# Optimization experiments

Hardware: AMD Instinct MI355X
Metric: run time of the kernel (lower is better)

## Reference

```python
import jax, jax.numpy as jnp
import numpy as np

B, L, H, NUM_LABELS = 4, 256, 768, 13


def setup_inputs() -> dict:
    key = jax.random.key(0)
    k1, k2, k3, k4, k5 = jax.random.split(key, 5)
    s1 = 1.0 / np.sqrt(2 * H)
    s2 = 1.0 / np.sqrt(H)
    return {
        "hidden_states": jax.random.normal(k1, (B, L, H), dtype=jnp.float32),
        "W1": jax.random.uniform(k2, (2 * H, H), jnp.float32, -s1, s1),
        "b1": jax.random.uniform(k3, (H,), jnp.float32, -s1, s1),
        "W2": jax.random.uniform(k4, (H, NUM_LABELS), jnp.float32, -s2, s2),
        "b2": jax.random.uniform(k5, (NUM_LABELS,), jnp.float32, -s2, s2),
    }


def reference(hidden_states, W1, b1, W2, b2):
    # Original: ffn(cat([x_start expand over dim2, x_end expand over dim1], -1))
    # Algebraically: Linear(2H->H) on the concat == proj(x_start) + proj(x_end)
    # broadcast over the L x L span grid, avoiding the (B,L,L,2H) tensor.
    H_ = hidden_states.shape[-1]
    xs_proj = jnp.einsum('bsh,hk->bsk', hidden_states, W1[:H_])   # start half
    xe_proj = jnp.einsum('bsh,hk->bsk', hidden_states, W1[H_:])   # end half
    h = xs_proj[:, :, None, :] + xe_proj[:, None, :, :] + b1      # (B,L,L,H)
    h = jax.nn.gelu(h, approximate=False)                         # torch GELU default = exact erf
    logits = jnp.einsum('bijk,kn->bijn', h, W2) + b2              # (B,L,L,num_labels)
    return logits
```

## Files before the change

### kernel.cpp

```cpp
#include <hip/hip_runtime.h>
#include <math.h>

#define H 768
#define L 256
#define NB 4
#define NL 13

typedef _Float16 h2 __attribute__((ext_vector_type(2)));
typedef _Float16 h4 __attribute__((ext_vector_type(4)));
typedef _Float16 half8 __attribute__((ext_vector_type(8)));
typedef float f32x4 __attribute__((ext_vector_type(4)));

__device__ inline unsigned int h2const(float f) {
    _Float16 c = (_Float16)f;
    h2 r = {c, c};
    return __builtin_bit_cast(unsigned int, r);
}

__device__ inline void gelu4_asm(
    unsigned int xs0, unsigned int xs1, unsigned int xs2, unsigned int xs3,
    unsigned int xe0, unsigned int xe1, unsigned int xe2, unsigned int xe3,
    unsigned int lo, unsigned int hi,
    unsigned int d4, unsigned int d3, unsigned int d2, unsigned int d1,
    unsigned int d0,
    unsigned int& o0r, unsigned int& o1r, unsigned int& o2r, unsigned int& o3r)
{
    unsigned int o0, o1, o2, o3, c0, c1, c2, c3, u0, u1, u2, u3, p0, p1, p2, p3;
    asm("v_pk_add_f16 %[o0], %[xs0], %[xe0]\n\t"
        "v_pk_add_f16 %[o1], %[xs1], %[xe1]\n\t"
        "v_pk_add_f16 %[o2], %[xs2], %[xe2]\n\t"
        "v_pk_add_f16 %[o3], %[xs3], %[xe3]\n\t"
        "v_pk_max_f16 %[c0], %[o0], %[lo]\n\t"
        "v_pk_max_f16 %[c1], %[o1], %[lo]\n\t"
        "v_pk_max_f16 %[c2], %[o2], %[lo]\n\t"
        "v_pk_max_f16 %[c3], %[o3], %[lo]\n\t"
        "v_pk_min_f16 %[c0], %[c0], %[hi]\n\t"
        "v_pk_min_f16 %[c1], %[c1], %[hi]\n\t"
        "v_pk_min_f16 %[c2], %[c2], %[hi]\n\t"
        "v_pk_min_f16 %[c3], %[c3], %[hi]\n\t"
        "v_pk_mul_f16 %[u0], %[c0], %[c0]\n\t"
        "v_pk_mul_f16 %[u1], %[c1], %[c1]\n\t"
        "v_pk_mul_f16 %[u2], %[c2], %[c2]\n\t"
        "v_pk_mul_f16 %[u3], %[c3], %[c3]\n\t"
        "v_pk_fma_f16 %[p0], %[u0], %[d4], %[d3]\n\t"
        "v_pk_fma_f16 %[p1], %[u1], %[d4], %[d3]\n\t"
        "v_pk_fma_f16 %[p2], %[u2], %[d4], %[d3]\n\t"
        "v_pk_fma_f16 %[p3], %[u3], %[d4], %[d3]\n\t"
        "v_pk_fma_f16 %[p0], %[u0], %[p0], %[d2]\n\t"
        "v_pk_fma_f16 %[p1], %[u1], %[p1], %[d2]\n\t"
        "v_pk_fma_f16 %[p2], %[u2], %[p2], %[d2]\n\t"
        "v_pk_fma_f16 %[p3], %[u3], %[p3], %[d2]\n\t"
        "v_pk_fma_f16 %[p0], %[u0], %[p0], %[d1]\n\t"
        "v_pk_fma_f16 %[p1], %[u1], %[p1], %[d1]\n\t"
        "v_pk_fma_f16 %[p2], %[u2], %[p2], %[d1]\n\t"
        "v_pk_fma_f16 %[p3], %[u3], %[p3], %[d1]\n\t"
        "v_pk_fma_f16 %[p0], %[u0], %[p0], %[d0]\n\t"
        "v_pk_fma_f16 %[p1], %[u1], %[p1], %[d0]\n\t"
        "v_pk_fma_f16 %[p2], %[u2], %[p2], %[d0]\n\t"
        "v_pk_fma_f16 %[p3], %[u3], %[p3], %[d0]\n\t"
        "v_pk_mul_f16 %[p0], %[c0], %[p0]\n\t"
        "v_pk_mul_f16 %[p1], %[c1], %[p1]\n\t"
        "v_pk_mul_f16 %[p2], %[c2], %[p2]\n\t"
        "v_pk_mul_f16 %[p3], %[c3], %[p3]\n\t"
        "v_pk_fma_f16 %[o0], %[o0], %[p0], %[o0]\n\t"
        "v_pk_fma_f16 %[o1], %[o1], %[p1], %[o1]\n\t"
        "v_pk_fma_f16 %[o2], %[o2], %[p2], %[o2]\n\t"
        "v_pk_fma_f16 %[o3], %[o3], %[p3], %[o3]"
        : [o0]"=&v"(o0), [o1]"=&v"(o1), [o2]"=&v"(o2), [o3]"=&v"(o3),
          [c0]"=&v"(c0), [c1]"=&v"(c1), [c2]"=&v"(c2), [c3]"=&v"(c3),
          [u0]"=&v"(u0), [u1]"=&v"(u1), [u2]"=&v"(u2), [u3]"=&v"(u3),
          [p0]"=&v"(p0), [p1]"=&v"(p1), [p2]"=&v"(p2), [p3]"=&v"(p3)
        : [xs0]"v"(xs0), [xs1]"v"(xs1), [xs2]"v"(xs2), [xs3]"v"(xs3),
          [xe0]"v"(xe0), [xe1]"v"(xe1), [xe2]"v"(xe2), [xe3]"v"(xe3),
          [lo]"v"(lo), [hi]"v"(hi), [d4]"v"(d4), [d3]"v"(d3),
          [d2]"v"(d2), [d1]"v"(d1), [d0]"v"(d0));
    o0r = o0; o1r = o1; o2r = o2; o3r = o3;
}

__global__ __launch_bounds__(256) void gemm_fused(
    const float* __restrict__ X, const float* __restrict__ W1,
    const float* __restrict__ b1, const float* __restrict__ W2,
    _Float16* __restrict__ Pxs2, _Float16* __restrict__ Pxe,
    _Float16* __restrict__ Bfrag2)
{
    const int tid = threadIdx.x;

    if (blockIdx.x >= 768) {
        int base = (blockIdx.x - 768) * 768 + tid;
        #pragma unroll
        for (int r = 0; r < 3; ++r) {
            int idx = base + r * 256;
            int u = idx & 7;
            int lane = (idx >> 3) & 63;
            int kb = idx >> 9;
            int k = kb * 32 + ((lane >> 4) << 3) + u;
            int nn = lane & 15;
            float v = (nn < NL) ? W2[(size_t)k * NL + nn] : 0.f;
            Bfrag2[idx] = (_Float16)(0.5f * v);
        }
        return;
    }

    __shared__ _Float16 As[2][32][72];
    __shared__ _Float16 Bs[2][64][72];

    const int w = tid >> 6, lane = tid & 63;
    const int ln = lane & 15, quad = lane >> 4;
    const int bm = blockIdx.x & 31;
    const int bn = blockIdx.x >> 5;
    const int m0 = bm * 32;
    const int n0g = bn * 64;
    const bool isE = (n0g >= H);
    const float* Wb = W1 + (isE ? (size_t)H * H : 0);
    const int c0 = isE ? (n0g - H) : n0g;

    const int ar = tid >> 4;
    const int ac = (tid & 15) * 4;

    float4 fA0, fA1, fB0a, fB0b, fB1a, fB1b;

#define G_LOAD(KR) do { \
    const int k0_ = (KR) * 64; \
    fA0 = *(const float4*)&X[(size_t)(m0 + ar) * H + k0_ + ac]; \
    fA1 = *(const float4*)&X[(size_t)(m0 + 16 + ar) * H + k0_ + ac]; \
    const float* wr0_ = &Wb[(size_t)(k0_ + 2 * ar) * H + c0 + ac]; \
    fB0a = *(const float4*)wr0_; \
    fB0b = *(const float4*)(wr0_ + H); \
    const float* wr1_ = &Wb[(size_t)(k0_ + 2 * (16 + ar)) * H + c0 + ac]; \
    fB1a = *(const float4*)wr1_; \
    fB1b = *(const float4*)(wr1_ + H); \
} while (0)

#define L_STORE(BUF) do { \
    h4 oa0 = { (_Float16)fA0.x, (_Float16)fA0.y, (_Float16)fA0.z, (_Float16)fA0.w }; \
    h4 oa1 = { (_Float16)fA1.x, (_Float16)fA1.y, (_Float16)fA1.z, (_Float16)fA1.w }; \
    *(h4*)&As[BUF][ar][ac] = oa0; \
    *(h4*)&As[BUF][16 + ar][ac] = oa1; \
    h2 p0 = {(_Float16)fB0a.x, (_Float16)fB0b.x}; \
    h2 p1 = {(_Float16)fB0a.y, (_Float16)fB0b.y}; \
    h2 p2 = {(_Float16)fB0a.z, (_Float16)fB0b.z}; \
    h2 p3 = {(_Float16)fB0a.w, (_Float16)fB0b.w}; \
    *(h2*)&Bs[BUF][ac + 0][2 * ar] = p0; \
    *(h2*)&Bs[BUF][ac + 1][2 * ar] = p1; \
    *(h2*)&Bs[BUF][ac + 2][2 * ar] = p2; \
    *(h2*)&Bs[BUF][ac + 3][2 * ar] = p3; \
    h2 q0 = {(_Float16)fB1a.x, (_Float16)fB1b.x}; \
    h2 q1 = {(_Float16)fB1a.y, (_Float16)fB1b.y}; \
    h2 q2 = {(_Float16)fB1a.z, (_Float16)fB1b.z}; \
    h2 q3 = {(_Float16)fB1a.w, (_Float16)fB1b.w}; \
    *(h2*)&Bs[BUF][ac + 0][2 * (16 + ar)] = q0; \
    *(h2*)&Bs[BUF][ac + 1][2 * (16 + ar)] = q1; \
    *(h2*)&Bs[BUF][ac + 2][2 * (16 + ar)] = q2; \
    *(h2*)&Bs[BUF][ac + 3][2 * (16 + ar)] = q3; \
} while (0)

    const int wm = w & 1, wn = w >> 1;
    f32x4 acc[2] = {};

    G_LOAD(0);
    L_STORE(0);
    __syncthreads();

    for (int kr = 0; kr < 12; ++kr) {
        const int cur = kr & 1;
        if (kr < 11) G_LOAD(kr + 1);
        #pragma unroll
        for (int sub = 0; sub < 2; ++sub) {
            const int ko = sub * 32 + quad * 8;
            half8 a   = *(const half8*)&As[cur][wm * 16 + ln][ko];
            half8 b0  = *(const half8*)&Bs[cur][wn * 32 + ln][ko];
            half8 b1f = *(const half8*)&Bs[cur][wn * 32 + 16 + ln][ko];
            acc[0] = __builtin_amdgcn_mfma_f32_16x16x32_f16(a, b0,  acc[0], 0, 0, 0);
            acc[1] = __builtin_amdgcn_mfma_f32_16x16x32_f16(a, b1f, acc[1], 0, 0, 0);
        }
        if (kr < 11) L_STORE(cur ^ 1);
        __syncthreads();
    }

    const int mb = m0 + wm * 16 + quad * 4;
    const int nb = wn * 32;
    if (!isE) {
        float bv0 = b1[n0g + nb + ln];
        float bv1 = b1[n0g + nb + 16 + ln];
        #pragma unroll
        for (int r = 0; r < 4; ++r) {
            Pxs2[(size_t)(mb + r) * H + (n0g + nb + ln)]      = (_Float16)(acc[0][r] + bv0);
            Pxs2[(size_t)(mb + r) * H + (n0g + nb + 16 + ln)] = (_Float16)(acc[1][r] + bv1);
        }
    } else {
        #pragma unroll
        for (int r = 0; r < 4; ++r) {
            Pxe[(size_t)(mb + r) * H + (c0 + nb + ln)]      = (_Float16)acc[0][r];
            Pxe[(size_t)(mb + r) * H + (c0 + nb + 16 + ln)] = (_Float16)acc[1][r];
        }
    }
#undef G_LOAD
#undef L_STORE
}

__global__ __launch_bounds__(256, 4) void span_mfma_kernel(
    const _Float16* __restrict__ Pxs2, const _Float16* __restrict__ Pxe,
    const _Float16* __restrict__ Bfrag2, const float* __restrict__ b2,
    float* __restrict__ out)
{
    __shared__ unsigned int xsf[4 * H / 2];
    const int ip = blockIdx.x >> 2;
    const int jq = blockIdx.x & 3;
    const int bi0 = ip * 4;
    const int b = bi0 >> 8;
    const int tid = threadIdx.x;

    const unsigned int* xsrc = (const unsigned int*)(Pxs2 + (size_t)bi0 * H);
    #pragma unroll
    for (int t = 0; t < 6; ++t) xsf[t * 256 + tid] = xsrc[t * 256 + tid];

    const int wave = tid >> 6;
    const int lane = tid & 63;
    const int n = lane & 15;
    const int quad = lane >> 4;
    const int j_load = jq * 64 + wave * 16 + n;

    const _Float16* xerow = Pxe + (size_t)(b * L + j_load) * H + quad * 8;
    const uint4* bptr = (const uint4*)(Bfrag2 + (size_t)lane * 8);

    unsigned int cLo = h2const(-3.75f), cHi = h2const(3.75f);
    unsigned int cD4 = h2const(2.0333e-5f), cD3 = h2const(-0.00084672f);
    unsigned int cD2 = h2const(0.0140002f), cD1 = h2const(-0.1234557f);
    unsigned int cD0 = h2const(0.7946463f);
    asm("" : "+v"(cLo), "+v"(cHi), "+v"(cD4), "+v"(cD3),
             "+v"(cD2), "+v"(cD1), "+v"(cD0));

    f32x4 acc[4] = {};
    __syncthreads();

    uint4 xe0 = *(const uint4*)(xerow);
    uint4 xe1 = *(const uint4*)(xerow + 32);
    uint4 bf0 = bptr[0];
    uint4 bf1 = bptr[64];

    const int xob = quad * 4;
    uint4 xa0 = *(const uint4*)&xsf[0 * (H / 2) + xob];
    uint4 xa1 = *(const uint4*)&xsf[1 * (H / 2) + xob];
    uint4 xa2 = *(const uint4*)&xsf[2 * (H / 2) + xob];
    uint4 xa3 = *(const uint4*)&xsf[3 * (H / 2) + xob];

    #pragma unroll 2
    for (int kb = 0; kb < H / 32; ++kb) {
        uint4 xecur = xe0;  xe0 = xe1;
        uint4 bfcur = bf0;  bf0 = bf1;
        if (kb < H / 32 - 2) {
            xe1 = *(const uint4*)(xerow + (kb + 2) * 32);
            bf1 = bptr[(kb + 2) * 64];
        }

        uint4 nx0 = xa0, nx1 = xa1, nx2 = xa2, nx3 = xa3;
        if (kb < H / 32 - 1) {
            const int xon = (kb + 1) * 16 + quad * 4;
            nx0 = *(const uint4*)&xsf[0 * (H / 2) + xon];
            nx1 = *(const uint4*)&xsf[1 * (H / 2) + xon];
            nx2 = *(const uint4*)&xsf[2 * (H / 2) + xon];
            nx3 = *(const uint4*)&xsf[3 * (H / 2) + xon];
        }

        half8 bfrag = __builtin_bit_cast(half8, bfcur);
        unsigned int pk0, pk1, pk2, pk3;

        gelu4_asm(xa0.x, xa0.y, xa0.z, xa0.w,
                  xecur.x, xecur.y, xecur.z, xecur.w,
                  cLo, cHi, cD4, cD3, cD2, cD1, cD0, pk0, pk1, pk2, pk3);
        { uint4 pk4 = {pk0, pk1, pk2, pk3};
          acc[0] = __builtin_amdgcn_mfma_f32_16x16x32_f16(
                       __builtin_bit_cast(half8, pk4), bfrag, acc[0], 0, 0, 0); }

        gelu4_asm(xa1.x, xa1.y, xa1.z, xa1.w,
                  xecur.x, xecur.y, xecur.z, xecur.w,
                  cLo, cHi, cD4, cD3, cD2, cD1, cD0, pk0, pk1, pk2, pk3);
        { uint4 pk4 = {pk0, pk1, pk2, pk3};
          acc[1] = __builtin_amdgcn_mfma_f32_16x16x32_f16(
                       __builtin_bit_cast(half8, pk4), bfrag, acc[1], 0, 0, 0); }

        gelu4_asm(xa2.x, xa2.y, xa2.z, xa2.w,
                  xecur.x, xecur.y, xecur.z, xecur.w,
                  cLo, cHi, cD4, cD3, cD2, cD1, cD0, pk0, pk1, pk2, pk3);
        { uint4 pk4 = {pk0, pk1, pk2, pk3};
          acc[2] = __builtin_amdgcn_mfma_f32_16x16x32_f16(
                       __builtin_bit_cast(half8, pk4), bfrag, acc[2], 0, 0, 0); }

        gelu4_asm(xa3.x, xa3.y, xa3.z, xa3.w,
                  xecur.x, xecur.y, xecur.z, xecur.w,
                  cLo, cHi, cD4, cD3, cD2, cD1, cD0, pk0, pk1, pk2, pk3);
        { uint4 pk4 = {pk0, pk1, pk2, pk3};
          acc[3] = __builtin_amdgcn_mfma_f32_16x16x32_f16(
                       __builtin_bit_cast(half8, pk4), bfrag, acc[3], 0, 0, 0); }

        xa0 = nx0; xa1 = nx1; xa2 = nx2; xa3 = nx3;
    }

    if (n < NL) {
        float b2v = b2[n];
        #pragma unroll
        for (int i01 = 0; i01 < 4; ++i01)
            #pragma unroll
            for (int r = 0; r < 4; ++r) {
                int j = jq * 64 + wave * 16 + quad * 4 + r;
                out[((size_t)(bi0 + i01) * L + j) * NL + n] = acc[i01][r] + b2v;
            }
    }
}

extern "C" void kernel_launch(void* const* d_in, const int* in_sizes, int n_in,
                              void* d_out, int out_size, void* d_ws, size_t ws_size,
                              hipStream_t stream)
{
    (void)in_sizes; (void)n_in; (void)out_size; (void)ws_size;
    const float* X  = (const float*)d_in[0];
    const float* W1 = (const float*)d_in[1];
    const float* b1 = (const float*)d_in[2];
    const float* W2 = (const float*)d_in[3];
    const float* b2 = (const float*)d_in[4];
    float* out = (float*)d_out;

    char* ws = (char*)d_ws;
    _Float16* Pxs2   = (_Float16*)ws;
    _Float16* Pxe    = Pxs2 + (size_t)NB * L * H;
    _Float16* Bfrag2 = Pxe + (size_t)NB * L * H;

    gemm_fused<<<dim3(784), 256, 0, stream>>>(X, W1, b1, W2, Pxs2, Pxe, Bfrag2);
    span_mfma_kernel<<<NB * L, 256, 0, stream>>>(Pxs2, Pxe, Bfrag2, b2, out);
}
```

Before: 119.5 us.

## Fuse GEMM and span kernels into one cooperative launch with grid sync

```diff
diff --git a/kernel.cpp b/kernel.cpp
--- a/kernel.cpp
+++ b/kernel.cpp
@@ -1,5 +1,8 @@
 #include <hip/hip_runtime.h>
+#include <hip/hip_cooperative_groups.h>
 #include <math.h>
+
+namespace cg = cooperative_groups;
 
 #define H 768
 #define L 256
@@ -77,47 +80,6 @@
     o0r = o0; o1r = o1; o2r = o2; o3r = o3;
 }
 
-__global__ __launch_bounds__(256) void gemm_fused(
-    const float* __restrict__ X, const float* __restrict__ W1,
-    const float* __restrict__ b1, const float* __restrict__ W2,
-    _Float16* __restrict__ Pxs2, _Float16* __restrict__ Pxe,
-    _Float16* __restrict__ Bfrag2)
-{
-    const int tid = threadIdx.x;
-
-    if (blockIdx.x >= 768) {
-        int base = (blockIdx.x - 768) * 768 + tid;
-        #pragma unroll
-        for (int r = 0; r < 3; ++r) {
-            int idx = base + r * 256;
-            int u = idx & 7;
-            int lane = (idx >> 3) & 63;
-            int kb = idx >> 9;
-            int k = kb * 32 + ((lane >> 4) << 3) + u;
-            int nn = lane & 15;
-            float v = (nn < NL) ? W2[(size_t)k * NL + nn] : 0.f;
-            Bfrag2[idx] = (_Float16)(0.5f * v);
-        }
-        return;
-    }
-
-    __shared__ _Float16 As[2][32][72];
-    __shared__ _Float16 Bs[2][64][72];
-
-    const int w = tid >> 6, lane = tid & 63;
-    const int ln = lane & 15, quad = lane >> 4;
-    const int bm = blockIdx.x & 31;
-    const int bn = blockIdx.x >> 5;
-    const int m0 = bm * 32;
-    const int n0g = bn * 64;
-    const bool isE = (n0g >= H);
-    const float* Wb = W1 + (isE ? (size_t)H * H : 0);
-    const int c0 = isE ? (n0g - H) : n0g;
-
-    const int ar = tid >> 4;
-    const int ac = (tid & 15) * 4;
-
-    float4 fA0, fA1, fB0a, fB0b, fB1a, fB1b;
 
 #define G_LOAD(KR) do { \
     const int k0_ = (KR) * 64; \
@@ -154,6 +116,45 @@
     *(h2*)&Bs[BUF][ac + 3][2 * (16 + ar)] = q3; \
 } while (0)
 
+__device__ __forceinline__ void gemm_phase(
+    int wid, int tid,
+    const float* __restrict__ X, const float* __restrict__ W1,
+    const float* __restrict__ b1, const float* __restrict__ W2,
+    _Float16* __restrict__ Pxs2, _Float16* __restrict__ Pxe,
+    _Float16* __restrict__ Bfrag2,
+    _Float16 (*As)[32][72], _Float16 (*Bs)[64][72])
+{
+    if (wid >= 768) {
+        int base = (wid - 768) * 768 + tid;
+        #pragma unroll
+        for (int r = 0; r < 3; ++r) {
+            int idx = base + r * 256;
+            int u = idx & 7;
+            int lane = (idx >> 3) & 63;
+            int kb = idx >> 9;
+            int k = kb * 32 + ((lane >> 4) << 3) + u;
+            int nn = lane & 15;
+            float v = (nn < NL) ? W2[(size_t)k * NL + nn] : 0.f;
+            Bfrag2[idx] = (_Float16)(0.5f * v);
+        }
+        return;
+    }
+
+    const int w = tid >> 6, lane = tid & 63;
+    const int ln = lane & 15, quad = lane >> 4;
+    const int bm = wid & 31;
+    const int bn = wid >> 5;
+    const int m0 = bm * 32;
+    const int n0g = bn * 64;
+    const bool isE = (n0g >= H);
+    const float* Wb = W1 + (isE ? (size_t)H * H : 0);
+    const int c0 = isE ? (n0g - H) : n0g;
+
+    const int ar = tid >> 4;
+    const int ac = (tid & 15) * 4;
+
+    float4 fA0, fA1, fB0a, fB0b, fB1a, fB1b;
+
     const int wm = w & 1, wn = w >> 1;
     f32x4 acc[2] = {};
 
@@ -194,21 +195,18 @@
             Pxe[(size_t)(mb + r) * H + (c0 + nb + 16 + ln)] = (_Float16)acc[1][r];
         }
     }
-#undef G_LOAD
-#undef L_STORE
-}
-
-__global__ __launch_bounds__(256, 4) void span_mfma_kernel(
+}
+
+__device__ __forceinline__ void span_phase(
+    int bid, int tid,
     const _Float16* __restrict__ Pxs2, const _Float16* __restrict__ Pxe,
     const _Float16* __restrict__ Bfrag2, const float* __restrict__ b2,
-    float* __restrict__ out)
-{
-    __shared__ unsigned int xsf[4 * H / 2];
-    const int ip = blockIdx.x >> 2;
-    const int jq = blockIdx.x & 3;
+    float* __restrict__ out, unsigned int* xsf)
+{
+    const int ip = bid >> 2;
+    const int jq = bid & 3;
     const int bi0 = ip * 4;
     const int b = bi0 >> 8;
-    const int tid = threadIdx.x;
 
     const unsigned int* xsrc = (const unsigned int*)(Pxs2 + (size_t)bi0 * H);
     #pragma unroll
@@ -308,6 +306,50 @@
     }
 }
 
+__global__ __launch_bounds__(256, 4) void fused_kernel(
+    const float* __restrict__ X, const float* __restrict__ W1,
+    const float* __restrict__ b1, const float* __restrict__ W2,
+    const float* __restrict__ b2,
+    _Float16* __restrict__ Pxs2, _Float16* __restrict__ Pxe,
+    _Float16* __restrict__ Bfrag2, float* __restrict__ out)
+{
+    __shared__ __align__(16) unsigned char smem[27648];
+    _Float16 (*As)[32][72] = reinterpret_cast<_Float16(*)[32][72]>(smem);
+    _Float16 (*Bs)[64][72] = reinterpret_cast<_Float16(*)[64][72]>(smem + 9216);
+    unsigned int* xsf = reinterpret_cast<unsigned int*>(smem);
+
+    const int tid = threadIdx.x;
+    const int bid = blockIdx.x;
+
+    if (bid < 784)
+        gemm_phase(bid, tid, X, W1, b1, W2, Pxs2, Pxe, Bfrag2, As, Bs);
+
+    cg::this_grid().sync();
+
+    span_phase(bid, tid, Pxs2, Pxe, Bfrag2, b2, out, xsf);
+}
+
+__global__ __launch_bounds__(256) void gemm_fused(
+    const float* __restrict__ X, const float* __restrict__ W1,
+    const float* __restrict__ b1, const float* __restrict__ W2,
+    _Float16* __restrict__ Pxs2, _Float16* __restrict__ Pxe,
+    _Float16* __restrict__ Bfrag2)
+{
+    __shared__ __align__(16) unsigned char smem[27648];
+    _Float16 (*As)[32][72] = reinterpret_cast<_Float16(*)[32][72]>(smem);
+    _Float16 (*Bs)[64][72] = reinterpret_cast<_Float16(*)[64][72]>(smem + 9216);
+    gemm_phase(blockIdx.x, threadIdx.x, X, W1, b1, W2, Pxs2, Pxe, Bfrag2, As, Bs);
+}
+
+__global__ __launch_bounds__(256, 4) void span_mfma_kernel(
+    const _Float16* __restrict__ Pxs2, const _Float16* __restrict__ Pxe,
+    const _Float16* __restrict__ Bfrag2, const float* __restrict__ b2,
+    float* __restrict__ out)
+{
+    __shared__ __align__(16) unsigned int xsf[4 * H / 2];
+    span_phase(blockIdx.x, threadIdx.x, Pxs2, Pxe, Bfrag2, b2, out, xsf);
+}
+
 extern "C" void kernel_launch(void* const* d_in, const int* in_sizes, int n_in,
                               void* d_out, int out_size, void* d_ws, size_t ws_size,
                               hipStream_t stream)
@@ -325,6 +367,12 @@
     _Float16* Pxe    = Pxs2 + (size_t)NB * L * H;
     _Float16* Bfrag2 = Pxe + (size_t)NB * L * H;
 
-    gemm_fused<<<dim3(784), 256, 0, stream>>>(X, W1, b1, W2, Pxs2, Pxe, Bfrag2);
-    span_mfma_kernel<<<NB * L, 256, 0, stream>>>(Pxs2, Pxe, Bfrag2, b2, out);
-}
+    void* args[] = { (void*)&X, (void*)&W1, (void*)&b1, (void*)&W2, (void*)&b2,
+                     (void*)&Pxs2, (void*)&Pxe, (void*)&Bfrag2, (void*)&out };
+    hipError_t err = hipLaunchCooperativeKernel(
+        (void*)fused_kernel, dim3(1024), dim3(256), args, 0, stream);
+    if (err != hipSuccess) {
+        gemm_fused<<<dim3(784), 256, 0, stream>>>(X, W1, b1, W2, Pxs2, Pxe, Bfrag2);
+        span_mfma_kernel<<<NB * L, 256, 0, stream>>>(Pxs2, Pxe, Bfrag2, b2, out);
+    }
+}
```

Result: slower. 267.4 us (+123.7%).
